# Kernel tuning notes

Hardware: AMD Instinct MI355X
Metric: run time of the kernel (lower is better)

The kernel has to match this reference:

```python
import jax, jax.numpy as jnp
import numpy as np

EPS_NORM = 1e-10
EPS_EXP = 1e-6


def setup_inputs() -> dict:
    key = jax.random.key(0)
    k1, k2 = jax.random.split(key)
    B, F, H, W = 16, 2048, 8, 8
    X = jax.random.normal(k1, (B, F, H, W), dtype=jnp.float32)
    M = jax.random.normal(k2, (B, F, H, W), dtype=jnp.float32)
    return {"X": X, "M": M}


def reference(X, M):
    B, F, H, W = X.shape
    N = H * W
    X = X.reshape(B, F, N)
    M = M.reshape(B, F, N)

    # feature centering over dim=-2 (the feature axis of (B, F, N))
    X = X - X.mean(axis=1, keepdims=True)
    M = M - M.mean(axis=1, keepdims=True)

    # feature_normalize: L2 norm over dim 1, keepdim, + eps
    X = X / (jnp.linalg.norm(X, axis=1, keepdims=True) + EPS_NORM)
    M = M / (jnp.linalg.norm(M, axis=1, keepdims=True) + EPS_NORM)

    # MatmulTopkLoss: S = X @ M^T over spatial N -> (B, F, F)
    S = jnp.einsum('bfn,bgn->bfg', X, M)
    YX = S + jnp.transpose(S, (0, 2, 1))  # symmetrize
    P = jax.nn.softmax(YX, axis=-1)

    k = F // 2
    value, idx = jax.lax.top_k(P, k)  # (B, F, k) values desc, indices
    value_sum = value.sum(axis=-1, keepdims=True)
    row_pos = jnp.arange(F)[None, :, None]  # (1, F, 1)
    dist = jnp.abs(idx - row_pos).astype(value.dtype)
    C_xy = (value * dist / value_sum).mean(axis=-1)  # (B, F)

    xy = jnp.exp(-C_xy + C_xy.min() - EPS_EXP)
    return jnp.reshape(xy.mean(), (1,))
```

## Files before the change

kernel.cpp:

```cpp
#include <hip/hip_runtime.h>
#include <hip/hip_bf16.h>
#include <math.h>

#define B_   16
#define F_   2048
#define N_   64
#define K_   1024
#define YP   2056

typedef short bf16x8 __attribute__((ext_vector_type(8)));
typedef float v4f    __attribute__((ext_vector_type(4)));

__device__ __forceinline__ float wave_sum(float v) {
#pragma unroll
  for (int off = 32; off > 0; off >>= 1) v += __shfl_down(v, off, 64);
  return v;
}
__device__ __forceinline__ float wave_max(float v) {
#pragma unroll
  for (int off = 32; off > 0; off >>= 1) v = fmaxf(v, __shfl_down(v, off, 64));
  return v;
}

__device__ __forceinline__ unsigned f2bf(float x) {
  const unsigned u = __float_as_uint(x);
  return (u + 0x7FFFu + ((u >> 16) & 1u)) >> 16;
}
__device__ __forceinline__ float bf2f(unsigned us) {
  return __uint_as_float(us << 16);
}
__device__ __forceinline__ unsigned ord2u16(unsigned T) {
  return (T & 0x8000u) ? (T ^ 0x8000u) : (T ^ 0xFFFFu);
}
__device__ __forceinline__ unsigned ordpair(unsigned wd) {
  return wd ^ (0x80008000u | (((wd & 0x80008000u) >> 15) * 0x7FFFu));
}

__global__ __launch_bounds__(256) void stats_kernel(
    const float* __restrict__ X, const float* __restrict__ M,
    float* __restrict__ P) {
  __shared__ float red[4][N_][4];
  const int tid = threadIdx.x;
  const int b = blockIdx.x >> 4;
  const int fb = blockIdx.x & 15;
  const int f0 = fb * 128;
  const int fi = tid >> 6, n = tid & 63;
  float sx = 0.f, sxx = 0.f, sm = 0.f, smm = 0.f;
#pragma unroll 4
  for (int j = 0; j < 32; ++j) {
    const int f = f0 + fi + 4 * j;
    const size_t gi = ((size_t)b * F_ + f) * N_ + n;
    const float x = X[gi];
    const float m = M[gi];
    sx += x; sxx += x * x; sm += m; smm += m * m;
  }
  red[fi][n][0] = sx; red[fi][n][1] = sxx;
  red[fi][n][2] = sm; red[fi][n][3] = smm;
  __syncthreads();
  const int wn = tid & 63, word = tid >> 6;
  const float s = red[0][wn][word] + red[1][wn][word] +
                  red[2][wn][word] + red[3][wn][word];
  P[(((size_t)b * N_ + wn) * 4 + word) * 16 + fb] = s;
}

__global__ __launch_bounds__(256) void normbf_kernel(
    const float* __restrict__ X, const float* __restrict__ M,
    const float* __restrict__ P,
    short* __restrict__ Xb16, short* __restrict__ Mb16) {
  const int tid = threadIdx.x;
  const int b = blockIdx.x >> 4;
  const int f0 = (blockIdx.x & 15) * 128;
  const int n = tid & 63;
  const float* base = P + (((size_t)b * N_ + n) * 4) * 16;
  float acc4[4];
#pragma unroll
  for (int wj = 0; wj < 4; ++wj) {
    float s = 0.f;
#pragma unroll
    for (int i = 0; i < 16; ++i) s += base[16 * wj + i];
    acc4[wj] = s;
  }
  const float sx = acc4[0], sxx = acc4[1], sm = acc4[2], smm = acc4[3];
  const float mux = sx * (1.f / F_), mum = sm * (1.f / F_);
  const float rx = 1.f / (sqrtf(fmaxf(sxx - (float)F_ * mux * mux, 0.f)) + 1e-10f);
  const float rm = 1.f / (sqrtf(fmaxf(smm - (float)F_ * mum * mum, 0.f)) + 1e-10f);
#pragma unroll 4
  for (int jj = 0; jj < 32; ++jj) {
    const int f = f0 + (tid >> 6) + 4 * jj;
    const size_t gi = ((size_t)b * F_ + f) * N_ + n;
    Xb16[gi] = (short)f2bf((X[gi] - mux) * rx);
    Mb16[gi] = (short)f2bf((M[gi] - mum) * rm);
  }
}

__global__ __launch_bounds__(512)
__attribute__((amdgpu_waves_per_eu(4, 4)))
void rows_kernel(
    const short* __restrict__ Xb16, const short* __restrict__ Mb16,
    float* __restrict__ C) {
  __shared__ unsigned short yxu[16 * YP];
  __shared__ unsigned histS[8 * 256];

  const int tid = threadIdx.x;
  const int w = tid >> 6, lane = tid & 63;
  const int nl = lane & 15, q = lane >> 4;
  const int b = blockIdx.x >> 7;
  const int f0 = (blockIdx.x & 127) * 16;
  const int g0 = 256 * w;

  const short* __restrict__ Xb = Xb16 + (size_t)b * F_ * N_;
  const short* __restrict__ Mb = Mb16 + (size_t)b * F_ * N_;

  const short* Ax = Xb + (size_t)(f0 + nl) * N_ + 8 * q;
  const short* Am = Mb + (size_t)(f0 + nl) * N_ + 8 * q;
  const bf16x8 ax0 = *(const bf16x8*)(Ax);
  const bf16x8 ax1 = *(const bf16x8*)(Ax + 32);
  const bf16x8 am0 = *(const bf16x8*)(Am);
  const bf16x8 am1 = *(const bf16x8*)(Am + 32);

  v4f acc[16];
#pragma unroll
  for (int t = 0; t < 16; ++t) acc[t] = (v4f)(0.f);

#pragma unroll
  for (int t = 0; t < 16; ++t) {
    const short* Bm = Mb + (size_t)(g0 + 16 * t + nl) * N_ + 8 * q;
    const short* Bx = Xb + (size_t)(g0 + 16 * t + nl) * N_ + 8 * q;
    const bf16x8 bm0 = *(const bf16x8*)(Bm);
    const bf16x8 bm1 = *(const bf16x8*)(Bm + 32);
    const bf16x8 bx0 = *(const bf16x8*)(Bx);
    const bf16x8 bx1 = *(const bf16x8*)(Bx + 32);
    acc[t] = __builtin_amdgcn_mfma_f32_16x16x32_bf16(ax0, bm0, acc[t], 0, 0, 0);
    acc[t] = __builtin_amdgcn_mfma_f32_16x16x32_bf16(ax1, bm1, acc[t], 0, 0, 0);
    acc[t] = __builtin_amdgcn_mfma_f32_16x16x32_bf16(am0, bx0, acc[t], 0, 0, 0);
    acc[t] = __builtin_amdgcn_mfma_f32_16x16x32_bf16(am1, bx1, acc[t], 0, 0, 0);
  }

#pragma unroll
  for (int t = 0; t < 16; ++t) {
    const int col = g0 + 16 * t + nl;
#pragma unroll
    for (int r = 0; r < 4; ++r)
      yxu[(4 * q + r) * YP + col] = (unsigned short)f2bf(acc[t][r]);
  }
  __syncthreads();

  unsigned* wh = &histS[w << 8];
#pragma unroll 1
  for (int r4 = 0; r4 < 2; ++r4) {
    const int row = 2 * w + r4;
    const int frow = f0 + row;
    const uint4* rp = (const uint4*)(yxu + row * YP);

    unsigned pk[16];
    unsigned kmin = 0xFFFFFFFFu, kmax = 0u;
#pragma unroll
    for (int j = 0; j < 4; ++j) {
      const uint4 tt = rp[lane + 64 * j];
      const unsigned wds[4] = {tt.x, tt.y, tt.z, tt.w};
#pragma unroll
      for (int c = 0; c < 4; ++c) {
        const unsigned o = ordpair(wds[c]);
        pk[4 * j + c] = o;
        const unsigned o0 = o & 0xFFFFu, o1 = o >> 16;
        kmin = min(kmin, min(o0, o1));
        kmax = max(kmax, max(o0, o1));
      }
    }
#pragma unroll
    for (int off = 32; off > 0; off >>= 1) {
      kmin = min(kmin, (unsigned)__shfl_down((int)kmin, off, 64));
      kmax = max(kmax, (unsigned)__shfl_down((int)kmax, off, 64));
    }
    kmin = (unsigned)__shfl((int)kmin, 0, 64);
    kmax = (unsigned)__shfl((int)kmax, 0, 64);

    unsigned lo = kmin, R = kmax - kmin, krem = K_;
    unsigned T, tie_need;
    if (R == 0) {
      T = lo; tie_need = krem;
    } else {
      for (;;) {
        const int pos = 31 - __builtin_clz(R);
        const int sh = (pos > 7) ? (pos - 7) : 0;
#pragma unroll
        for (int i = 0; i < 4; ++i) wh[lane + 64 * i] = 0u;
        __builtin_amdgcn_wave_barrier();
#pragma unroll
        for (int c = 0; c < 16; ++c) {
          const unsigned o = pk[c];
          const unsigned d0 = (o & 0xFFFFu) - lo;
          const unsigned d1 = (o >> 16) - lo;
          if (d0 <= R) atomicAdd(&wh[d0 >> sh], 1u);
          if (d1 <= R) atomicAdd(&wh[d1 >> sh], 1u);
        }
        __builtin_amdgcn_wave_barrier();
        unsigned h[4];
#pragma unroll
        for (int i = 0; i < 4; ++i) h[i] = wh[4 * lane + i];
        unsigned s3 = h[3], s2 = h[2] + s3, s1 = h[1] + s2, s0 = h[0] + s1;
        unsigned tot = s0;
#pragma unroll
        for (int off = 1; off < 64; off <<= 1) {
          const unsigned v = __shfl_down(tot, off, 64);
          if (lane + off < 64) tot += v;
        }
        const unsigned above = tot - s0;
        const unsigned S[4] = {above + s0, above + s1, above + s2, above + s3};
        unsigned packed = 0;
        bool found = false;
#pragma unroll
        for (int i = 0; i < 4; ++i) {
          const unsigned Sip1 = S[i] - h[i];
          if (S[i] >= krem && Sip1 < krem) {
            packed = ((unsigned)(4 * lane + i) << 16) | Sip1;
            found = true;
          }
        }
        const unsigned long long bm = __ballot(found);
        const int winner = __ffsll(bm) - 1;
        packed = (unsigned)__shfl((int)packed, winner, 64);
        const unsigned D = packed >> 16;
        krem -= (packed & 0xFFFFu);
        if (sh == 0) { T = lo + D; tie_need = krem; break; }
        lo += (D << sh);
        R = (1u << sh) - 1u;
      }
    }

    float vs = 0.f, ws = 0.f;
    unsigned cnt[4];
#pragma unroll
    for (int j = 0; j < 4; ++j) {
      cnt[j] = 0;
#pragma unroll
      for (int c = 0; c < 4; ++c) {
        const unsigned o = pk[4 * j + c];
        const unsigned oo[2] = {o & 0xFFFFu, o >> 16};
#pragma unroll
        for (int i = 0; i < 2; ++i) {
          const int g = 512 * j + 8 * lane + 2 * c + i;
          if (oo[i] > T) {
            const float pv = __expf(bf2f(ord2u16(oo[i])));
            vs += pv; ws += pv * fabsf((float)(g - frow));
          } else if (oo[i] == T) cnt[j]++;
        }
      }
    }
    const float ptie = __expf(bf2f(ord2u16(T)));

    unsigned pA = cnt[0] | (cnt[1] << 16), pB = cnt[2] | (cnt[3] << 16);
    unsigned iA = pA, iB = pB;
#pragma unroll
    for (int off = 1; off < 64; off <<= 1) {
      const unsigned vA = __shfl_up(iA, off, 64);
      const unsigned vB = __shfl_up(iB, off, 64);
      if (lane >= off) { iA += vA; iB += vB; }
    }
    const unsigned eA = iA - pA, eB = iB - pB;
    const unsigned tA = (unsigned)__shfl((int)iA, 63, 64);
    const unsigned tB = (unsigned)__shfl((int)iB, 63, 64);
    unsigned G[4];
    G[0] = 0;
    G[1] = G[0] + (tA & 0xFFFFu);
    G[2] = G[1] + (tA >> 16);
    G[3] = G[2] + (tB & 0xFFFFu);
#pragma unroll
    for (int j = 0; j < 4; ++j) {
      if (cnt[j]) {
        const unsigned off = (j < 2) ? ((eA >> (16 * j)) & 0xFFFFu)
                                     : ((eB >> (16 * (j - 2))) & 0xFFFFu);
        unsigned cc = 0;
#pragma unroll
        for (int c = 0; c < 4; ++c) {
          const unsigned o = pk[4 * j + c];
          const unsigned oo[2] = {o & 0xFFFFu, o >> 16};
#pragma unroll
          for (int i = 0; i < 2; ++i) {
            if (oo[i] == T) {
              if (G[j] + off + cc < tie_need) {
                const int g = 512 * j + 8 * lane + 2 * c + i;
                vs += ptie; ws += ptie * fabsf((float)(g - frow));
              }
              cc++;
            }
          }
        }
      }
    }

    vs = wave_sum(vs); ws = wave_sum(ws);
    if (lane == 0)
      C[(size_t)b * F_ + frow] = (ws / vs) * (1.f / (float)K_);
  }
}

__global__ __launch_bounds__(1024) void final_kernel(
    const float* __restrict__ C, unsigned* __restrict__ out) {
  __shared__ float red[16];
  const int tid = threadIdx.x;
  const int wave = tid >> 6, lane = tid & 63;
  float v[32];
  float mn = 3.4e38f;
#pragma unroll
  for (int i = 0; i < 32; ++i) {
    v[i] = C[tid + 1024 * i];
    mn = fminf(mn, v[i]);
  }
  mn = -wave_max(-mn);
  if (lane == 0) red[wave] = mn;
  __syncthreads();
  float cmin = red[0];
  for (int w = 1; w < 16; ++w) cmin = fminf(cmin, red[w]);
  __syncthreads();
  float s = 0.f;
#pragma unroll
  for (int i = 0; i < 32; ++i) s += expf(cmin - v[i] - 1e-6f);
  s = wave_sum(s);
  if (lane == 0) red[wave] = s;
  __syncthreads();
  if (tid == 0) {
    float tot = 0.f;
    for (int w = 0; w < 16; ++w) tot += red[w];
    const float res = tot * (1.f / 32768.f);
    const __hip_bfloat16 hb = __float2bfloat16(res);
    const unsigned short u = *(const unsigned short*)&hb;
    out[0] = ((unsigned)u << 16) | (unsigned)u;
  }
}

extern "C" void kernel_launch(void* const* d_in, const int* in_sizes, int n_in,
                              void* d_out, int out_size, void* d_ws, size_t ws_size,
                              hipStream_t stream) {
  const float* X = (const float*)d_in[0];
  const float* M = (const float*)d_in[1];
  short* Xb16 = (short*)d_ws;
  short* Mb16 = Xb16 + (size_t)B_ * F_ * N_;
  float* C = (float*)(Mb16 + (size_t)B_ * F_ * N_);
  float* P = C + (size_t)B_ * F_;

  stats_kernel<<<dim3(B_ * 16), dim3(256), 0, stream>>>(X, M, P);
  normbf_kernel<<<dim3(B_ * 16), dim3(256), 0, stream>>>(X, M, P, Xb16, Mb16);
  rows_kernel<<<dim3(B_ * (F_ / 16)), dim3(512), 0, stream>>>(Xb16, Mb16, C);
  final_kernel<<<dim3(1), dim3(1024), 0, stream>>>(C, (unsigned*)d_out);
}
```

Baseline: 231.8 us.

## Split fused rows kernel into MFMA YX kernel and per-row radix select kernel

```diff
diff --git a/kernel.cpp b/kernel.cpp
--- a/kernel.cpp
+++ b/kernel.cpp
@@ -93,6 +93,193 @@
   }
 }
 
+__global__ __launch_bounds__(512) void yx_kernel(
+    const short* __restrict__ Xb16, const short* __restrict__ Mb16,
+    unsigned short* __restrict__ YXg, int blk0) {
+  const int tid = threadIdx.x;
+  const int w = tid >> 6, lane = tid & 63;
+  const int nl = lane & 15, q = lane >> 4;
+  const int bid = blockIdx.x + blk0;
+  const int b = bid >> 7;
+  const int f0 = (bid & 127) * 16;
+  const int g0 = 256 * w;
+
+  const short* __restrict__ Xb = Xb16 + (size_t)b * F_ * N_;
+  const short* __restrict__ Mb = Mb16 + (size_t)b * F_ * N_;
+
+  const short* Ax = Xb + (size_t)(f0 + nl) * N_ + 8 * q;
+  const short* Am = Mb + (size_t)(f0 + nl) * N_ + 8 * q;
+  const bf16x8 ax0 = *(const bf16x8*)(Ax);
+  const bf16x8 ax1 = *(const bf16x8*)(Ax + 32);
+  const bf16x8 am0 = *(const bf16x8*)(Am);
+  const bf16x8 am1 = *(const bf16x8*)(Am + 32);
+
+  v4f acc[16];
+#pragma unroll
+  for (int t = 0; t < 16; ++t) acc[t] = (v4f)(0.f);
+
+#pragma unroll
+  for (int t = 0; t < 16; ++t) {
+    const short* Bm = Mb + (size_t)(g0 + 16 * t + nl) * N_ + 8 * q;
+    const short* Bx = Xb + (size_t)(g0 + 16 * t + nl) * N_ + 8 * q;
+    const bf16x8 bm0 = *(const bf16x8*)(Bm);
+    const bf16x8 bm1 = *(const bf16x8*)(Bm + 32);
+    const bf16x8 bx0 = *(const bf16x8*)(Bx);
+    const bf16x8 bx1 = *(const bf16x8*)(Bx + 32);
+    acc[t] = __builtin_amdgcn_mfma_f32_16x16x32_bf16(ax0, bm0, acc[t], 0, 0, 0);
+    acc[t] = __builtin_amdgcn_mfma_f32_16x16x32_bf16(ax1, bm1, acc[t], 0, 0, 0);
+    acc[t] = __builtin_amdgcn_mfma_f32_16x16x32_bf16(am0, bx0, acc[t], 0, 0, 0);
+    acc[t] = __builtin_amdgcn_mfma_f32_16x16x32_bf16(am1, bx1, acc[t], 0, 0, 0);
+  }
+
+  unsigned short* out =
+      YXg + (size_t)(blockIdx.x * 16 + 4 * q) * F_;
+#pragma unroll
+  for (int t = 0; t < 16; ++t) {
+    const int col = g0 + 16 * t + nl;
+#pragma unroll
+    for (int r = 0; r < 4; ++r)
+      out[(size_t)r * F_ + col] = (unsigned short)f2bf(acc[t][r]);
+  }
+}
+
+__global__ __launch_bounds__(256) void select_kernel(
+    const unsigned short* __restrict__ YXg, float* __restrict__ C,
+    int rowbase) {
+  __shared__ unsigned histS[4 * 256];
+  const int tid = threadIdx.x;
+  const int w = tid >> 6, lane = tid & 63;
+  const int lrow = blockIdx.x * 4 + w;
+  const int grow = rowbase + lrow;
+  const int frow = grow & (F_ - 1);
+
+  const uint4* rp = (const uint4*)(YXg + (size_t)lrow * F_);
+  unsigned* wh = &histS[w << 8];
+
+  unsigned pk[16];
+#pragma unroll
+  for (int j = 0; j < 4; ++j) {
+    const uint4 tt = rp[lane + 64 * j];
+    const unsigned wds[4] = {tt.x, tt.y, tt.z, tt.w};
+#pragma unroll
+    for (int c = 0; c < 4; ++c) pk[4 * j + c] = ordpair(wds[c]);
+  }
+
+  unsigned lo = 0, R = 0xFFFFu, krem = K_;
+  unsigned T, tie_need;
+  for (;;) {
+    const int pos = 31 - __builtin_clz(R);
+    const int sh = (pos > 7) ? (pos - 7) : 0;
+#pragma unroll
+    for (int i = 0; i < 4; ++i) wh[lane + 64 * i] = 0u;
+    __builtin_amdgcn_wave_barrier();
+#pragma unroll
+    for (int c = 0; c < 16; ++c) {
+      const unsigned o = pk[c];
+      const unsigned d0 = (o & 0xFFFFu) - lo;
+      const unsigned d1 = (o >> 16) - lo;
+      if (d0 <= R) atomicAdd(&wh[d0 >> sh], 1u);
+      if (d1 <= R) atomicAdd(&wh[d1 >> sh], 1u);
+    }
+    __builtin_amdgcn_wave_barrier();
+    unsigned h[4];
+#pragma unroll
+    for (int i = 0; i < 4; ++i) h[i] = wh[4 * lane + i];
+    unsigned s3 = h[3], s2 = h[2] + s3, s1 = h[1] + s2, s0 = h[0] + s1;
+    unsigned tot = s0;
+#pragma unroll
+    for (int off = 1; off < 64; off <<= 1) {
+      const unsigned v = __shfl_down(tot, off, 64);
+      if (lane + off < 64) tot += v;
+    }
+    const unsigned above = tot - s0;
+    const unsigned S[4] = {above + s0, above + s1, above + s2, above + s3};
+    unsigned packed = 0;
+    bool found = false;
+#pragma unroll
+    for (int i = 0; i < 4; ++i) {
+      const unsigned Sip1 = S[i] - h[i];
+      if (S[i] >= krem && Sip1 < krem) {
+        packed = ((unsigned)(4 * lane + i) << 16) | Sip1;
+        found = true;
+      }
+    }
+    const unsigned long long bm = __ballot(found);
+    const int winner = __ffsll(bm) - 1;
+    packed = (unsigned)__shfl((int)packed, winner, 64);
+    const unsigned D = packed >> 16;
+    krem -= (packed & 0xFFFFu);
+    if (sh == 0) { T = lo + D; tie_need = krem; break; }
+    lo += (D << sh);
+    R = (1u << sh) - 1u;
+  }
+
+  float vs = 0.f, ws = 0.f;
+  unsigned cnt[4];
+#pragma unroll
+  for (int j = 0; j < 4; ++j) {
+    cnt[j] = 0;
+#pragma unroll
+    for (int c = 0; c < 4; ++c) {
+      const unsigned o = pk[4 * j + c];
+      const unsigned oo[2] = {o & 0xFFFFu, o >> 16};
+#pragma unroll
+      for (int i = 0; i < 2; ++i) {
+        const int g = 512 * j + 8 * lane + 2 * c + i;
+        if (oo[i] > T) {
+          const float pv = __expf(bf2f(ord2u16(oo[i])));
+          vs += pv; ws += pv * fabsf((float)(g - frow));
+        } else if (oo[i] == T) cnt[j]++;
+      }
+    }
+  }
+  const float ptie = __expf(bf2f(ord2u16(T)));
+
+  unsigned pA = cnt[0] | (cnt[1] << 16), pB = cnt[2] | (cnt[3] << 16);
+  unsigned iA = pA, iB = pB;
+#pragma unroll
+  for (int off = 1; off < 64; off <<= 1) {
+    const unsigned vA = __shfl_up(iA, off, 64);
+    const unsigned vB = __shfl_up(iB, off, 64);
+    if (lane >= off) { iA += vA; iB += vB; }
+  }
+  const unsigned eA = iA - pA, eB = iB - pB;
+  const unsigned tA = (unsigned)__shfl((int)iA, 63, 64);
+  const unsigned tB = (unsigned)__shfl((int)iB, 63, 64);
+  unsigned G[4];
+  G[0] = 0;
+  G[1] = G[0] + (tA & 0xFFFFu);
+  G[2] = G[1] + (tA >> 16);
+  G[3] = G[2] + (tB & 0xFFFFu);
+#pragma unroll
+  for (int j = 0; j < 4; ++j) {
+    if (cnt[j]) {
+      const unsigned off = (j < 2) ? ((eA >> (16 * j)) & 0xFFFFu)
+                                   : ((eB >> (16 * (j - 2))) & 0xFFFFu);
+      unsigned cc = 0;
+#pragma unroll
+      for (int c = 0; c < 4; ++c) {
+        const unsigned o = pk[4 * j + c];
+        const unsigned oo[2] = {o & 0xFFFFu, o >> 16};
+#pragma unroll
+        for (int i = 0; i < 2; ++i) {
+          if (oo[i] == T) {
+            if (G[j] + off + cc < tie_need) {
+              const int g = 512 * j + 8 * lane + 2 * c + i;
+              vs += ptie; ws += ptie * fabsf((float)(g - frow));
+            }
+            cc++;
+          }
+        }
+      }
+    }
+  }
+
+  vs = wave_sum(vs); ws = wave_sum(ws);
+  if (lane == 0)
+    C[grow] = (ws / vs) * (1.f / (float)K_);
+}
+
 __global__ __launch_bounds__(512)
 __attribute__((amdgpu_waves_per_eu(4, 4)))
 void rows_kernel(
@@ -338,9 +525,26 @@
   short* Mb16 = Xb16 + (size_t)B_ * F_ * N_;
   float* C = (float*)(Mb16 + (size_t)B_ * F_ * N_);
   float* P = C + (size_t)B_ * F_;
+  unsigned short* YXg = (unsigned short*)(P + (size_t)B_ * N_ * 4 * 16);
+  const size_t base_bytes = (size_t)(8 * 1024 * 1024) + 128 * 1024 + 512 * 1024 + 64 * 1024;
 
   stats_kernel<<<dim3(B_ * 16), dim3(256), 0, stream>>>(X, M, P);
   normbf_kernel<<<dim3(B_ * 16), dim3(256), 0, stream>>>(X, M, P, Xb16, Mb16);
-  rows_kernel<<<dim3(B_ * (F_ / 16)), dim3(512), 0, stream>>>(Xb16, Mb16, C);
+
+  const int total_blk = B_ * (F_ / 16);
+  const size_t blk_bytes = (size_t)16 * F_ * 2;
+  int cb = 0;
+  if (ws_size > base_bytes + blk_bytes)
+    cb = (int)((ws_size - base_bytes) / blk_bytes);
+  if (cb < 1) {
+    rows_kernel<<<dim3(total_blk), dim3(512), 0, stream>>>(Xb16, Mb16, C);
+  } else {
+    if (cb > total_blk) cb = total_blk;
+    for (int s = 0; s < total_blk; s += cb) {
+      const int nb = (s + cb <= total_blk) ? cb : (total_blk - s);
+      yx_kernel<<<dim3(nb), dim3(512), 0, stream>>>(Xb16, Mb16, YXg, s);
+      select_kernel<<<dim3(nb * 4), dim3(256), 0, stream>>>(YXg, C, s * 16);
+    }
+  }
   final_kernel<<<dim3(1), dim3(1024), 0, stream>>>(C, (unsigned*)d_out);
 }
```

Result: slower. 310.0 us (+33.7%).
